# Optimization experiments

Measured on AMD Instinct MI355X. Metric: run time of the kernel, lower is better.

The kernel has to match this reference:

```python
import jax, jax.numpy as jnp
import numpy as np
import math

N = 262144   # number of voxels (MHA batch dim, batch_first=True)
T = 1        # tgt_len (one query per voxel)
S = 9        # src_len (9 shifted-grid neighbors)
E = 32       # embed_dim
H = 2        # num_heads
HD = E // H  # head_dim = 16
SIGMA = 10.0 # hardcoded in gauss_MultiheadAttention.__init__


def setup_inputs() -> dict:
    key0 = jax.random.key(0)
    ks = jax.random.split(key0, 8)
    query = jax.random.normal(ks[0], (N, T, E), dtype=jnp.float32)
    key_t = jax.random.normal(ks[1], (N, S, E), dtype=jnp.float32)
    value = jax.random.normal(ks[2], (N, S, E), dtype=jnp.float32)
    gauss = jax.random.uniform(ks[3], (N, S), dtype=jnp.float32)  # nonneg squared-distance-like
    # packed in-projection weight [3E, E] (xavier_uniform) and zero bias, as in _reset_parameters
    limit = math.sqrt(6.0 / (3 * E + E))
    in_proj_weight = jax.random.uniform(ks[4], (3 * E, E), dtype=jnp.float32, minval=-limit, maxval=limit)
    in_proj_bias = jnp.zeros((3 * E,), dtype=jnp.float32)
    lim_o = math.sqrt(1.0 / E)
    out_proj_weight = jax.random.uniform(ks[5], (E, E), dtype=jnp.float32, minval=-lim_o, maxval=lim_o)
    out_proj_bias = jnp.zeros((E,), dtype=jnp.float32)
    return {
        "query": query, "key": key_t, "value": value, "gauss": gauss,
        "in_proj_weight": in_proj_weight, "in_proj_bias": in_proj_bias,
        "out_proj_weight": out_proj_weight, "out_proj_bias": out_proj_bias,
    }


def reference(query, key, value, gauss, in_proj_weight, in_proj_bias,
              out_proj_weight, out_proj_bias):
    # q/k/v in-projection (packed weight chunked in 3, q is not k so chunk path)
    w_q, w_k, w_v = in_proj_weight[:E], in_proj_weight[E:2 * E], in_proj_weight[2 * E:]
    b_q, b_k, b_v = in_proj_bias[:E], in_proj_bias[E:2 * E], in_proj_bias[2 * E:]
    q = jnp.einsum('bte,fe->btf', query, w_q) + b_q   # [N,T,E]
    k = jnp.einsum('bse,fe->bsf', key, w_k) + b_k     # [N,S,E]
    v = jnp.einsum('bse,fe->bsf', value, w_v) + b_v   # [N,S,E]
    # split heads: [N, len, H, HD] -> [N, H, len, HD]
    q = q.reshape(N, T, H, HD).transpose(0, 2, 1, 3)
    k = k.reshape(N, S, H, HD).transpose(0, 2, 1, 3)
    v = v.reshape(N, S, H, HD).transpose(0, 2, 1, 3)
    # scaled dot product; scale by sqrt(head_dim) (E in the kernel = per-head dim)
    q = q / math.sqrt(HD)
    attn = jnp.einsum('bhtd,bhsd->bhts', q, k)        # [N,H,T,S]
    # multiplicative gaussian reweighting applied to every head (even+odd rows)
    gauss_weight = jnp.exp(-gauss * SIGMA)[:, None, None, :]  # [N,1,1,S]
    attn = attn * gauss_weight
    attn = jax.nn.softmax(attn, axis=-1)
    # dropout_p=0 (eval-mode reference; dropout is stochastic)
    out = jnp.einsum('bhts,bhsd->bhtd', attn, v)      # [N,H,T,HD]
    out = out.transpose(0, 2, 1, 3).reshape(N, T, E)  # merge heads
    out = jnp.einsum('bte,fe->btf', out, out_proj_weight) + out_proj_bias
    return out
```

## Files before the change

### kernel.cpp

```cpp
#include <hip/hip_runtime.h>
#include <math.h>

#define SS 9
#define EE 32
#define TPB 256
#define PADW 33

#define WS_M0   0
#define WS_PT0  2048
#define WS_UB   4096
#define WS_U    4160
#define WS_BO2  4224
#define WS_C    4256

__global__ void gauss_prep_kernel(const float* __restrict__ ipw,
                                  const float* __restrict__ ipb,
                                  const float* __restrict__ opw,
                                  const float* __restrict__ opb,
                                  float* __restrict__ dw) {
  const int tid = threadIdx.x;
  for (int idx = tid; idx < 2048; idx += TPB) {
    const int h = idx >> 10, e = (idx >> 5) & 31, e2 = idx & 31;
    float acc = 0.f;
    for (int d = 0; d < 16; ++d)
      acc += ipw[(h * 16 + d) * 32 + e] * ipw[(32 + h * 16 + d) * 32 + e2];
    dw[WS_M0 + idx] = 0.25f * acc;
  }
  for (int idx = tid; idx < 2048; idx += TPB) {
    const int h = idx >> 10, e = (idx >> 5) & 31, f = idx & 31;
    float acc = 0.f;
    for (int d = 0; d < 16; ++d)
      acc += opw[f * 32 + h * 16 + d] * ipw[(64 + h * 16 + d) * 32 + e];
    dw[WS_PT0 + idx] = acc;
  }
  if (tid < 64) {
    const int h = tid >> 5, e = tid & 31;
    float a_ub = 0.f, a_u = 0.f;
    for (int d = 0; d < 16; ++d) {
      a_ub += ipb[h * 16 + d] * ipw[(32 + h * 16 + d) * 32 + e];
      a_u  += ipw[(h * 16 + d) * 32 + e] * ipb[32 + h * 16 + d];
    }
    dw[WS_UB + tid] = 0.25f * a_ub;
    dw[WS_U + tid]  = 0.25f * a_u;
  } else if (tid < 96) {
    const int f = tid - 64;
    float acc = opb[f];
    for (int j = 0; j < 32; ++j) acc += ipb[64 + j] * opw[f * 32 + j];
    dw[WS_BO2 + f] = acc;
  } else if (tid < 98) {
    const int h = tid - 96;
    float acc = 0.f;
    for (int d = 0; d < 16; ++d) acc += ipb[h * 16 + d] * ipb[32 + h * 16 + d];
    dw[WS_C + h] = 0.25f * acc;
  }
}

__global__ __launch_bounds__(TPB) void gauss_attn_kernel(
    const float* __restrict__ query,
    const float* __restrict__ key,
    const float* __restrict__ value,
    const float* __restrict__ gauss,
    const float* __restrict__ dw,
    float* __restrict__ out) {
  __shared__ float tile[TPB * PADW];
  __shared__ float gtile[TPB * SS];

  const int tid = threadIdx.x;
  const long b0 = (long)blockIdx.x * TPB;

  {
    const float* g = gauss + b0 * SS;
    for (int i = tid; i < TPB * SS; i += TPB) gtile[i] = g[i];
  }
  {
    const float4* q4 = (const float4*)(query + b0 * EE);
    #pragma unroll
    for (int i = 0; i < 8; ++i) {
      const int idx = i * TPB + tid;
      const float4 v = q4[idx];
      const int r = idx >> 3, j = idx & 7;
      float* t = &tile[r * PADW + 4 * j];
      t[0] = v.x; t[1] = v.y; t[2] = v.z; t[3] = v.w;
    }
  }
  __syncthreads();

  float qreg[32];
  #pragma unroll
  for (int e = 0; e < 32; ++e) qreg[e] = tile[tid * PADW + e];

  float gw[SS];
  #pragma unroll
  for (int s = 0; s < SS; ++s) gw[s] = __expf(-10.0f * gtile[tid * SS + s]);

  float t00 = dw[WS_C + 0], t01 = dw[WS_C + 1];
  #pragma unroll
  for (int e = 0; e < 32; ++e) {
    t00 += qreg[e] * dw[WS_U + e];
    t01 += qreg[e] * dw[WS_U + 32 + e];
  }

  float wv0[32], wv1[32];
  #pragma unroll
  for (int e2 = 0; e2 < 32; ++e2) {
    wv0[e2] = dw[WS_UB + e2];
    wv1[e2] = dw[WS_UB + 32 + e2];
  }
  #pragma unroll
  for (int e = 0; e < 32; ++e) {
    const float qe = qreg[e];
    #pragma unroll
    for (int e2 = 0; e2 < 32; ++e2) {
      wv0[e2] += qe * dw[WS_M0 + e * 32 + e2];
      wv1[e2] += qe * dw[WS_M0 + 1024 + e * 32 + e2];
    }
  }

  float qk0[SS], qk1[SS];
  #pragma unroll
  for (int s = 0; s < SS; ++s) {
    __syncthreads();
    #pragma unroll
    for (int i = 0; i < 8; ++i) {
      const int idx = i * TPB + tid;
      const int r = idx >> 3, j = idx & 7;
      const float4 v =
          *(const float4*)(key + (b0 + r) * (long)(SS * EE) + s * EE + 4 * j);
      float* t = &tile[r * PADW + 4 * j];
      t[0] = v.x; t[1] = v.y; t[2] = v.z; t[3] = v.w;
    }
    __syncthreads();
    float a0 = t00, a1 = t01;
    #pragma unroll
    for (int e = 0; e < 32; ++e) {
      const float kv = tile[tid * PADW + e];
      a0 += wv0[e] * kv;
      a1 += wv1[e] * kv;
    }
    qk0[s] = a0; qk1[s] = a1;
  }

  float p0[SS], p1[SS];
  {
    float m0 = -1e30f, m1 = -1e30f;
    #pragma unroll
    for (int s = 0; s < SS; ++s) {
      qk0[s] *= gw[s]; qk1[s] *= gw[s];
      m0 = fmaxf(m0, qk0[s]); m1 = fmaxf(m1, qk1[s]);
    }
    float l0 = 0.f, l1 = 0.f;
    #pragma unroll
    for (int s = 0; s < SS; ++s) {
      p0[s] = __expf(qk0[s] - m0); l0 += p0[s];
      p1[s] = __expf(qk1[s] - m1); l1 += p1[s];
    }
    const float r0 = 1.f / l0, r1 = 1.f / l1;
    #pragma unroll
    for (int s = 0; s < SS; ++s) { p0[s] *= r0; p1[s] *= r1; }
  }

  float vb0[32], vb1[32];
  #pragma unroll
  for (int e = 0; e < 32; ++e) { vb0[e] = 0.f; vb1[e] = 0.f; }
  #pragma unroll
  for (int s = 0; s < SS; ++s) {
    __syncthreads();
    #pragma unroll
    for (int i = 0; i < 8; ++i) {
      const int idx = i * TPB + tid;
      const int r = idx >> 3, j = idx & 7;
      const float4 v =
          *(const float4*)(value + (b0 + r) * (long)(SS * EE) + s * EE + 4 * j);
      float* t = &tile[r * PADW + 4 * j];
      t[0] = v.x; t[1] = v.y; t[2] = v.z; t[3] = v.w;
    }
    __syncthreads();
    const float w0 = p0[s], w1 = p1[s];
    #pragma unroll
    for (int e = 0; e < 32; ++e) {
      const float vv = tile[tid * PADW + e];
      vb0[e] += w0 * vv;
      vb1[e] += w1 * vv;
    }
  }

  float o[32];
  #pragma unroll
  for (int f = 0; f < 32; ++f) o[f] = dw[WS_BO2 + f];
  #pragma unroll
  for (int e = 0; e < 32; ++e) {
    const float x0 = vb0[e], x1 = vb1[e];
    #pragma unroll
    for (int f = 0; f < 32; ++f) {
      o[f] += x0 * dw[WS_PT0 + e * 32 + f];
      o[f] += x1 * dw[WS_PT0 + 1024 + e * 32 + f];
    }
  }

  __syncthreads();
  #pragma unroll
  for (int f = 0; f < 32; ++f) tile[tid * PADW + f] = o[f];
  __syncthreads();
  {
    float4* o4 = (float4*)(out + b0 * EE);
    #pragma unroll
    for (int i = 0; i < 8; ++i) {
      const int idx = i * TPB + tid;
      const int r = idx >> 3, j = idx & 7;
      const float* t = &tile[r * PADW + 4 * j];
      o4[idx] = make_float4(t[0], t[1], t[2], t[3]);
    }
  }
}

extern "C" void kernel_launch(void* const* d_in, const int* in_sizes, int n_in,
                              void* d_out, int out_size, void* d_ws, size_t ws_size,
                              hipStream_t stream) {
  const float* query = (const float*)d_in[0];
  const float* key   = (const float*)d_in[1];
  const float* value = (const float*)d_in[2];
  const float* gauss = (const float*)d_in[3];
  const float* ipw   = (const float*)d_in[4];
  const float* ipb   = (const float*)d_in[5];
  const float* opw   = (const float*)d_in[6];
  const float* opb   = (const float*)d_in[7];
  float* out = (float*)d_out;
  float* dw  = (float*)d_ws;

  const int n = in_sizes[0] / EE;
  gauss_prep_kernel<<<1, TPB, 0, stream>>>(ipw, ipb, opw, opb, dw);
  gauss_attn_kernel<<<n / TPB, TPB, 0, stream>>>(query, key, value, gauss, dw, out);
}
```

Before: 645.5 us.

## Load query/key/value directly per thread, drop LDS staging and barriers

The attention kernel no longer stages query, key, value, gauss and output through a padded shared-memory tile with barriers. Each thread now reads its own voxel's rows with float4 loads straight from global memory and writes its output directly. This removes the LDS traffic and the __syncthreads between the 9 key and 9 value steps. In exchange, each warp's accesses are strided by a full row (128 B for q/out, 1152 B for k/v), so they are not coalesced. The prep kernel also caches its weights in shared memory and unrolls its small loops.

```diff
diff --git a/kernel.cpp b/kernel.cpp
--- a/kernel.cpp
+++ b/kernel.cpp
@@ -4,7 +4,6 @@
 #define SS 9
 #define EE 32
 #define TPB 256
-#define PADW 33
 
 #define WS_M0   0
 #define WS_PT0  2048
@@ -18,39 +17,54 @@
                                   const float* __restrict__ opw,
                                   const float* __restrict__ opb,
                                   float* __restrict__ dw) {
+  __shared__ float s_ipw[3072];
+  __shared__ float s_opw[1024];
+  __shared__ float s_ipb[96];
+  __shared__ float s_opb[32];
   const int tid = threadIdx.x;
+  for (int i = tid; i < 3072; i += TPB) s_ipw[i] = ipw[i];
+  for (int i = tid; i < 1024; i += TPB) s_opw[i] = opw[i];
+  if (tid < 96) s_ipb[tid] = ipb[tid];
+  else if (tid < 128) s_opb[tid - 96] = opb[tid - 96];
+  __syncthreads();
+
   for (int idx = tid; idx < 2048; idx += TPB) {
     const int h = idx >> 10, e = (idx >> 5) & 31, e2 = idx & 31;
     float acc = 0.f;
+    #pragma unroll
     for (int d = 0; d < 16; ++d)
-      acc += ipw[(h * 16 + d) * 32 + e] * ipw[(32 + h * 16 + d) * 32 + e2];
+      acc += s_ipw[(h * 16 + d) * 32 + e] * s_ipw[(32 + h * 16 + d) * 32 + e2];
     dw[WS_M0 + idx] = 0.25f * acc;
   }
   for (int idx = tid; idx < 2048; idx += TPB) {
     const int h = idx >> 10, e = (idx >> 5) & 31, f = idx & 31;
     float acc = 0.f;
+    #pragma unroll
     for (int d = 0; d < 16; ++d)
-      acc += opw[f * 32 + h * 16 + d] * ipw[(64 + h * 16 + d) * 32 + e];
+      acc += s_opw[f * 32 + h * 16 + d] * s_ipw[(64 + h * 16 + d) * 32 + e];
     dw[WS_PT0 + idx] = acc;
   }
   if (tid < 64) {
     const int h = tid >> 5, e = tid & 31;
     float a_ub = 0.f, a_u = 0.f;
+    #pragma unroll
     for (int d = 0; d < 16; ++d) {
-      a_ub += ipb[h * 16 + d] * ipw[(32 + h * 16 + d) * 32 + e];
-      a_u  += ipw[(h * 16 + d) * 32 + e] * ipb[32 + h * 16 + d];
+      a_ub += s_ipb[h * 16 + d] * s_ipw[(32 + h * 16 + d) * 32 + e];
+      a_u  += s_ipw[(h * 16 + d) * 32 + e] * s_ipb[32 + h * 16 + d];
     }
     dw[WS_UB + tid] = 0.25f * a_ub;
     dw[WS_U + tid]  = 0.25f * a_u;
   } else if (tid < 96) {
     const int f = tid - 64;
-    float acc = opb[f];
-    for (int j = 0; j < 32; ++j) acc += ipb[64 + j] * opw[f * 32 + j];
+    float acc = s_opb[f];
+    #pragma unroll
+    for (int j = 0; j < 32; ++j) acc += s_ipb[64 + j] * s_opw[f * 32 + j];
     dw[WS_BO2 + f] = acc;
   } else if (tid < 98) {
     const int h = tid - 96;
     float acc = 0.f;
-    for (int d = 0; d < 16; ++d) acc += ipb[h * 16 + d] * ipb[32 + h * 16 + d];
+    #pragma unroll
+    for (int d = 0; d < 16; ++d) acc += s_ipb[h * 16 + d] * s_ipb[32 + h * 16 + d];
     dw[WS_C + h] = 0.25f * acc;
   }
 }
@@ -62,36 +76,25 @@
     const float* __restrict__ gauss,
     const float* __restrict__ dw,
     float* __restrict__ out) {
-  __shared__ float tile[TPB * PADW];
-  __shared__ float gtile[TPB * SS];
-
-  const int tid = threadIdx.x;
-  const long b0 = (long)blockIdx.x * TPB;
-
-  {
-    const float* g = gauss + b0 * SS;
-    for (int i = tid; i < TPB * SS; i += TPB) gtile[i] = g[i];
-  }
-  {
-    const float4* q4 = (const float4*)(query + b0 * EE);
+  const long b = (long)blockIdx.x * TPB + threadIdx.x;
+
+  float qreg[32];
+  {
+    const float4* q4 = (const float4*)(query + b * EE);
     #pragma unroll
     for (int i = 0; i < 8; ++i) {
-      const int idx = i * TPB + tid;
-      const float4 v = q4[idx];
-      const int r = idx >> 3, j = idx & 7;
-      float* t = &tile[r * PADW + 4 * j];
-      t[0] = v.x; t[1] = v.y; t[2] = v.z; t[3] = v.w;
-    }
-  }
-  __syncthreads();
-
-  float qreg[32];
-  #pragma unroll
-  for (int e = 0; e < 32; ++e) qreg[e] = tile[tid * PADW + e];
+      const float4 t = q4[i];
+      qreg[4 * i + 0] = t.x; qreg[4 * i + 1] = t.y;
+      qreg[4 * i + 2] = t.z; qreg[4 * i + 3] = t.w;
+    }
+  }
 
   float gw[SS];
-  #pragma unroll
-  for (int s = 0; s < SS; ++s) gw[s] = __expf(-10.0f * gtile[tid * SS + s]);
+  {
+    const float* g = gauss + b * SS;
+    #pragma unroll
+    for (int s = 0; s < SS; ++s) gw[s] = __expf(-10.0f * g[s]);
+  }
 
   float t00 = dw[WS_C + 0], t01 = dw[WS_C + 1];
   #pragma unroll
@@ -117,27 +120,26 @@
   }
 
   float qk0[SS], qk1[SS];
-  #pragma unroll
-  for (int s = 0; s < SS; ++s) {
-    __syncthreads();
-    #pragma unroll
-    for (int i = 0; i < 8; ++i) {
-      const int idx = i * TPB + tid;
-      const int r = idx >> 3, j = idx & 7;
-      const float4 v =
-          *(const float4*)(key + (b0 + r) * (long)(SS * EE) + s * EE + 4 * j);
-      float* t = &tile[r * PADW + 4 * j];
-      t[0] = v.x; t[1] = v.y; t[2] = v.z; t[3] = v.w;
-    }
-    __syncthreads();
-    float a0 = t00, a1 = t01;
-    #pragma unroll
-    for (int e = 0; e < 32; ++e) {
-      const float kv = tile[tid * PADW + e];
-      a0 += wv0[e] * kv;
-      a1 += wv1[e] * kv;
-    }
-    qk0[s] = a0; qk1[s] = a1;
+  {
+    const float4* k4 = (const float4*)(key + b * (long)(SS * EE));
+    #pragma unroll
+    for (int s = 0; s < SS; ++s) {
+      float kr[32];
+      #pragma unroll
+      for (int i = 0; i < 8; ++i) {
+        const float4 t = k4[s * 8 + i];
+        kr[4 * i + 0] = t.x; kr[4 * i + 1] = t.y;
+        kr[4 * i + 2] = t.z; kr[4 * i + 3] = t.w;
+      }
+      float a0 = t00, a1 = t01;
+      #pragma unroll
+      for (int e = 0; e < 32; ++e) {
+        a0 += wv0[e] * kr[e];
+        a1 += wv1[e] * kr[e];
+      }
+      qk0[s] = a0 * gw[s];
+      qk1[s] = a1 * gw[s];
+    }
   }
 
   float p0[SS], p1[SS];
@@ -145,7 +147,6 @@
     float m0 = -1e30f, m1 = -1e30f;
     #pragma unroll
     for (int s = 0; s < SS; ++s) {
-      qk0[s] *= gw[s]; qk1[s] *= gw[s];
       m0 = fmaxf(m0, qk0[s]); m1 = fmaxf(m1, qk1[s]);
     }
     float l0 = 0.f, l1 = 0.f;
@@ -162,25 +163,23 @@
   float vb0[32], vb1[32];
   #pragma unroll
   for (int e = 0; e < 32; ++e) { vb0[e] = 0.f; vb1[e] = 0.f; }
-  #pragma unroll
-  for (int s = 0; s < SS; ++s) {
-    __syncthreads();
-    #pragma unroll
-    for (int i = 0; i < 8; ++i) {
-      const int idx = i * TPB + tid;
-      const int r = idx >> 3, j = idx & 7;
-      const float4 v =
-          *(const float4*)(value + (b0 + r) * (long)(SS * EE) + s * EE + 4 * j);
-      float* t = &tile[r * PADW + 4 * j];
-      t[0] = v.x; t[1] = v.y; t[2] = v.z; t[3] = v.w;
-    }
-    __syncthreads();
-    const float w0 = p0[s], w1 = p1[s];
-    #pragma unroll
-    for (int e = 0; e < 32; ++e) {
-      const float vv = tile[tid * PADW + e];
-      vb0[e] += w0 * vv;
-      vb1[e] += w1 * vv;
+  {
+    const float4* v4 = (const float4*)(value + b * (long)(SS * EE));
+    #pragma unroll
+    for (int s = 0; s < SS; ++s) {
+      float vr[32];
+      #pragma unroll
+      for (int i = 0; i < 8; ++i) {
+        const float4 t = v4[s * 8 + i];
+        vr[4 * i + 0] = t.x; vr[4 * i + 1] = t.y;
+        vr[4 * i + 2] = t.z; vr[4 * i + 3] = t.w;
+      }
+      const float w0 = p0[s], w1 = p1[s];
+      #pragma unroll
+      for (int e = 0; e < 32; ++e) {
+        vb0[e] += w0 * vr[e];
+        vb1[e] += w1 * vr[e];
+      }
     }
   }
 
@@ -197,19 +196,11 @@
     }
   }
 
-  __syncthreads();
-  #pragma unroll
-  for (int f = 0; f < 32; ++f) tile[tid * PADW + f] = o[f];
-  __syncthreads();
-  {
-    float4* o4 = (float4*)(out + b0 * EE);
-    #pragma unroll
-    for (int i = 0; i < 8; ++i) {
-      const int idx = i * TPB + tid;
-      const int r = idx >> 3, j = idx & 7;
-      const float* t = &tile[r * PADW + 4 * j];
-      o4[idx] = make_float4(t[0], t[1], t[2], t[3]);
-    }
+  {
+    float4* o4 = (float4*)(out + b * EE);
+    #pragma unroll
+    for (int i = 0; i < 8; ++i)
+      o4[i] = make_float4(o[4 * i + 0], o[4 * i + 1], o[4 * i + 2], o[4 * i + 3]);
   }
 }
 
```

Measured after the change: 865.5 us. +34.1%, slower.
